# Kernel optimization log

Hardware: AMD Instinct MI355X
Metric: run time of the kernel (lower is better)

## Reference

```python
import jax, jax.numpy as jnp
import numpy as np


def setup_inputs() -> dict:
    key = jax.random.key(0)
    x = jax.random.normal(key, (16384, 4096), dtype=jnp.float32)
    return {"x": x, "k": 64}


def reference(x, k):
    # allow_negative_topk=False -> select and output based on ReLU(x)
    scores = jax.nn.relu(x)                      # [N, D]
    kk = min(k, scores.shape[-1])
    _, topk_idx = jax.lax.top_k(scores, kk)      # [N, kk]
    rows = jnp.arange(scores.shape[0])[:, None]  # [N, 1]
    mask = jnp.zeros_like(scores).at[rows, topk_idx].set(1.0)
    return scores * mask
```

## Files before the change

### kernel.cpp

```cpp
#include <hip/hip_runtime.h>


constexpr int ROW_LEN = 4096;
constexpr int TPB     = 256;
constexpr int SEG     = 128;
constexpr unsigned int KPRE_BITS = 0x3FC00000u;
constexpr unsigned int KMAX_BITS = 0x40C00000u;

typedef float f32x4 __attribute__((ext_vector_type(4)));

__global__ __launch_bounds__(TPB, 4)
void topk_relu_kernel(const float* __restrict__ x, const int* __restrict__ kptr,
                      float* __restrict__ out, int rows)
{
    __shared__ alignas(16) int hist[256];
    __shared__ unsigned int cand[4 * SEG];
    __shared__ int scnt[4];
    __shared__ unsigned int wmax[4];
    __shared__ unsigned int selT;
    __shared__ int selNeed, selAmb;
    __shared__ unsigned long long wtot64[4];
    __shared__ int sel_digit, sel_kk, sel_eq, sel_flag;

    const int row = blockIdx.x;
    if (row >= rows) return;
    const int tid  = threadIdx.x;
    const int lane = tid & 63;
    const int wid  = tid >> 6;

    int k = *kptr;
    if (k > ROW_LEN) k = ROW_LEN;

    const float* __restrict__ xrow = x + (size_t)row * ROW_LEN;
    unsigned int key[16];
#pragma unroll
    for (int j = 0; j < 4; ++j) {
        f32x4 v = *(const f32x4*)(xrow + j * 1024 + tid * 4);
#pragma unroll
        for (int c = 0; c < 4; ++c)
            key[4 * j + c] = __float_as_uint(fmaxf(v[c], 0.0f));
    }

    unsigned int mx = 0u;
#pragma unroll
    for (int j = 0; j < 16; ++j) mx = key[j] > mx ? key[j] : mx;
#pragma unroll
    for (int d = 1; d < 64; d <<= 1) {
        unsigned int o = __shfl_xor(mx, d);
        mx = o > mx ? o : mx;
    }
    int base = 0;
#pragma unroll
    for (int j = 0; j < 16; ++j) {
        const bool p = key[j] > KPRE_BITS;
        const unsigned long long mask = __ballot(p);
        const int prior = __builtin_amdgcn_mbcnt_hi(
            (unsigned int)(mask >> 32),
            __builtin_amdgcn_mbcnt_lo((unsigned int)mask, 0));
        const int idx = base + prior;
        if (p && idx < SEG) cand[(wid << 7) + idx] = key[j] - KPRE_BITS;
        base += (int)__popcll(mask);
    }
    if (lane == 0) { scnt[wid] = base; wmax[wid] = mx; }
    __syncthreads();

    const int c0 = scnt[0], c1 = scnt[1], c2 = scnt[2], c3 = scnt[3];
    const int cnt = c0 + c1 + c2 + c3;
    const bool segok = (c0 <= SEG) & (c1 <= SEG) & (c2 <= SEG) & (c3 <= SEG);
    unsigned int bmax = wmax[0];
    bmax = wmax[1] > bmax ? wmax[1] : bmax;
    bmax = wmax[2] > bmax ? wmax[2] : bmax;
    bmax = wmax[3] > bmax ? wmax[3] : bmax;

    unsigned int T;
    int need, amb;

    if (cnt >= k && segok && bmax < KMAX_BITS) {
        if (wid == 0) {
            const int sc[4] = {c0, c1, c2, c3};
            unsigned int c[8];
#pragma unroll
            for (int i = 0; i < 8; ++i) {
                const int s   = i >> 1;
                const int off = lane + 64 * (i & 1);
                c[i] = (off < sc[s]) ? cand[(s << 7) + off] : 0u;
            }
            int kk = k;
            int eqv = 0;
            unsigned int prefix = 0;
#pragma unroll
            for (int p = 0; p < 3; ++p) {
                const int shift = 16 - 8 * p;
                ((int4*)hist)[lane] = make_int4(0, 0, 0, 0);
#pragma unroll
                for (int i = 0; i < 8; ++i) {
                    const unsigned int ci = c[i];
                    if (ci != 0u && (p == 0 || (ci >> (shift + 8)) == prefix))
                        atomicAdd(&hist[(ci >> shift) & 255u], 1);
                }
                const int4 h = ((const int4*)hist)[lane];
                const int h0 = h.x, h1 = h.y, h2 = h.z, h3 = h.w;
                const int lsum = h0 + h1 + h2 + h3;
                int suf = lsum;
#pragma unroll
                for (int d = 1; d < 64; d <<= 1) {
                    int v = __shfl_down(suf, d);
                    if (lane < 64 - d) suf += v;
                }
                const unsigned long long mm = __ballot(suf >= kk);
                const int L = 63 - __clzll(mm);
                int dig = 0, kkn = 0, eqn = 0;
                if (lane == L) {
                    int cum = suf - lsum;
                    const int hh[4] = {h0, h1, h2, h3};
#pragma unroll
                    for (int b = 3; b >= 0; --b) {
                        if (cum + hh[b] >= kk) { dig = lane * 4 + b; kkn = kk - cum; eqn = hh[b]; break; }
                        cum += hh[b];
                    }
                }
                dig = __shfl(dig, L);
                kk  = __shfl(kkn, L);
                eqv = __shfl(eqn, L);
                prefix = (prefix << 8) | (unsigned int)dig;
            }
            if (lane == 0) {
                selT    = prefix + KPRE_BITS;
                selNeed = kk;
                selAmb  = (eqv != kk);
            }
        }
        __syncthreads();
        T    = selT;
        need = selNeed;
        amb  = selAmb;
    } else {
        int kk = k;
        unsigned int prefix = 0;
        int t0 = 0;
        for (int p = 0; p < 4; ++p) {
            const int shift = 24 - 8 * p;
            hist[tid] = 0;
            if (tid == 0) sel_flag = 0;
            __syncthreads();
#pragma unroll
            for (int j = 0; j < 16; ++j) {
                const unsigned int kj = key[j];
                if (kj != 0u && (p == 0 || (kj >> (shift + 8)) == prefix))
                    atomicAdd(&hist[(kj >> shift) & 255u], 1);
            }
            __syncthreads();
            if (tid < 64) {
                const int b0 = tid * 4;
                const int h0 = hist[b0 + 0], h1 = hist[b0 + 1];
                const int h2 = hist[b0 + 2], h3 = hist[b0 + 3];
                const int lsum = h0 + h1 + h2 + h3;
                int suf = lsum;
#pragma unroll
                for (int d = 1; d < 64; d <<= 1) {
                    int v = __shfl_down(suf, d);
                    if (lane < 64 - d) suf += v;
                }
                const unsigned long long mm = __ballot(suf >= kk);
                if (mm == 0ull) {
                    if (lane == 0) sel_flag = 1;
                } else {
                    const int L = 63 - __clzll(mm);
                    if (lane == L) {
                        int cum = suf - lsum;
                        const int hh[4] = {h0, h1, h2, h3};
#pragma unroll
                        for (int b = 3; b >= 0; --b) {
                            if (cum + hh[b] >= kk) {
                                sel_digit = b0 + b; sel_kk = kk - cum; sel_eq = hh[b]; break;
                            }
                            cum += hh[b];
                        }
                    }
                }
            }
            __syncthreads();
            if (sel_flag) { t0 = 1; break; }
            prefix = (prefix << 8) | (unsigned int)sel_digit;
            kk = sel_kk;
            __syncthreads();
        }
        if (t0) { T = 0u; need = 0; amb = 1; }
        else    { T = prefix; need = kk; amb = (sel_eq != kk); }
    }

    float* __restrict__ orow = out + (size_t)row * ROW_LEN;

    if (!amb) {
#pragma unroll
        for (int j = 0; j < 4; ++j) {
            f32x4 v;
#pragma unroll
            for (int c2 = 0; c2 < 4; ++c2) {
                const unsigned int kj = key[4 * j + c2];
                v[c2] = (kj >= T && T != 0u) ? __uint_as_float(kj) : 0.0f;
            }
            *(f32x4*)(orow + j * 1024 + tid * 4) = v;
        }
    } else {
        unsigned long long packed = 0ull;
#pragma unroll
        for (int j = 0; j < 4; ++j) {
            int e = 0;
#pragma unroll
            for (int c = 0; c < 4; ++c) e += (key[4 * j + c] == T) ? 1 : 0;
            packed |= (unsigned long long)e << (16 * j);
        }
        unsigned long long incp = packed;
#pragma unroll
        for (int d = 1; d < 64; d <<= 1) {
            unsigned long long v = __shfl_up(incp, d);
            if (lane >= d) incp += v;
        }
        if (lane == 63) wtot64[wid] = incp;
        __syncthreads();
        unsigned long long b64 = 0ull;
        for (int w = 0; w < wid; ++w) b64 += wtot64[w];
        const unsigned long long exclp = b64 + incp - packed;
        const unsigned long long t64 = wtot64[0] + wtot64[1] + wtot64[2] + wtot64[3];
        int S[4];
        S[0] = 0;
        S[1] = (int)(t64 & 0xFFFFull);
        S[2] = S[1] + (int)((t64 >> 16) & 0xFFFFull);
        S[3] = S[2] + (int)((t64 >> 32) & 0xFFFFull);
#pragma unroll
        for (int j = 0; j < 4; ++j) {
            int rr = S[j] + (int)((exclp >> (16 * j)) & 0xFFFFull);
            f32x4 v;
#pragma unroll
            for (int c2 = 0; c2 < 4; ++c2) {
                const unsigned int kj = key[4 * j + c2];
                const bool eq = (kj == T);
                const bool keep = (kj > T) || (eq && rr < need);
                v[c2] = keep ? __uint_as_float(kj) : 0.0f;
                rr += eq ? 1 : 0;
            }
            *(f32x4*)(orow + j * 1024 + tid * 4) = v;
        }
    }
}

extern "C" void kernel_launch(void* const* d_in, const int* in_sizes, int n_in,
                              void* d_out, int out_size, void* d_ws, size_t ws_size,
                              hipStream_t stream)
{
    const float* x    = (const float*)d_in[0];
    const int*   kptr = (const int*)d_in[1];
    float*       out  = (float*)d_out;
    const int rows = in_sizes[0] / ROW_LEN;
    topk_relu_kernel<<<rows, TPB, 0, stream>>>(x, kptr, out, rows);
}
```

Before: 101.2 us.

## Process two rows per block with early prefetch and lighter LDS barriers

Each block now handles two rows. Both rows are loaded into registers up front so the second row's global load overlaps the first row's selection. The per-row logic is moved into a device function sharing one LDS struct. __syncthreads is replaced by a custom barrier that waits only on lgkmcnt before s_barrier. The cost is higher register pressure from 32 keys per thread under launch_bounds(256,4), half as many blocks, and a weaker barrier that no longer waits on outstanding global stores.

```diff
diff --git a/kernel.cpp b/kernel.cpp
--- a/kernel.cpp
+++ b/kernel.cpp
@@ -9,38 +9,26 @@
 
 typedef float f32x4 __attribute__((ext_vector_type(4)));
 
-__global__ __launch_bounds__(TPB, 4)
-void topk_relu_kernel(const float* __restrict__ x, const int* __restrict__ kptr,
-                      float* __restrict__ out, int rows)
+__device__ __forceinline__ void bar_lds() {
+    asm volatile("s_waitcnt lgkmcnt(0)" ::: "memory");
+    __builtin_amdgcn_sched_barrier(0);
+    __builtin_amdgcn_s_barrier();
+}
+
+struct Shm {
+    alignas(16) int hist[256];
+    unsigned int cand[4 * SEG];
+    int scnt[4];
+    unsigned int wmax[4];
+    unsigned int selT;
+    int selNeed, selAmb;
+    unsigned long long wtot64[4];
+    int sel_digit, sel_kk, sel_eq, sel_flag;
+};
+
+__device__ __forceinline__ void topk_row(unsigned int (&key)[16], float* __restrict__ orow,
+                                         int k, int tid, int lane, int wid, Shm& s)
 {
-    __shared__ alignas(16) int hist[256];
-    __shared__ unsigned int cand[4 * SEG];
-    __shared__ int scnt[4];
-    __shared__ unsigned int wmax[4];
-    __shared__ unsigned int selT;
-    __shared__ int selNeed, selAmb;
-    __shared__ unsigned long long wtot64[4];
-    __shared__ int sel_digit, sel_kk, sel_eq, sel_flag;
-
-    const int row = blockIdx.x;
-    if (row >= rows) return;
-    const int tid  = threadIdx.x;
-    const int lane = tid & 63;
-    const int wid  = tid >> 6;
-
-    int k = *kptr;
-    if (k > ROW_LEN) k = ROW_LEN;
-
-    const float* __restrict__ xrow = x + (size_t)row * ROW_LEN;
-    unsigned int key[16];
-#pragma unroll
-    for (int j = 0; j < 4; ++j) {
-        f32x4 v = *(const f32x4*)(xrow + j * 1024 + tid * 4);
-#pragma unroll
-        for (int c = 0; c < 4; ++c)
-            key[4 * j + c] = __float_as_uint(fmaxf(v[c], 0.0f));
-    }
-
     unsigned int mx = 0u;
 #pragma unroll
     for (int j = 0; j < 16; ++j) mx = key[j] > mx ? key[j] : mx;
@@ -58,19 +46,19 @@
             (unsigned int)(mask >> 32),
             __builtin_amdgcn_mbcnt_lo((unsigned int)mask, 0));
         const int idx = base + prior;
-        if (p && idx < SEG) cand[(wid << 7) + idx] = key[j] - KPRE_BITS;
+        if (p && idx < SEG) s.cand[(wid << 7) + idx] = key[j] - KPRE_BITS;
         base += (int)__popcll(mask);
     }
-    if (lane == 0) { scnt[wid] = base; wmax[wid] = mx; }
-    __syncthreads();
-
-    const int c0 = scnt[0], c1 = scnt[1], c2 = scnt[2], c3 = scnt[3];
+    if (lane == 0) { s.scnt[wid] = base; s.wmax[wid] = mx; }
+    bar_lds();
+
+    const int c0 = s.scnt[0], c1 = s.scnt[1], c2 = s.scnt[2], c3 = s.scnt[3];
     const int cnt = c0 + c1 + c2 + c3;
     const bool segok = (c0 <= SEG) & (c1 <= SEG) & (c2 <= SEG) & (c3 <= SEG);
-    unsigned int bmax = wmax[0];
-    bmax = wmax[1] > bmax ? wmax[1] : bmax;
-    bmax = wmax[2] > bmax ? wmax[2] : bmax;
-    bmax = wmax[3] > bmax ? wmax[3] : bmax;
+    unsigned int bmax = s.wmax[0];
+    bmax = s.wmax[1] > bmax ? s.wmax[1] : bmax;
+    bmax = s.wmax[2] > bmax ? s.wmax[2] : bmax;
+    bmax = s.wmax[3] > bmax ? s.wmax[3] : bmax;
 
     unsigned int T;
     int need, amb;
@@ -81,9 +69,9 @@
             unsigned int c[8];
 #pragma unroll
             for (int i = 0; i < 8; ++i) {
-                const int s   = i >> 1;
+                const int sgi = i >> 1;
                 const int off = lane + 64 * (i & 1);
-                c[i] = (off < sc[s]) ? cand[(s << 7) + off] : 0u;
+                c[i] = (off < sc[sgi]) ? s.cand[(sgi << 7) + off] : 0u;
             }
             int kk = k;
             int eqv = 0;
@@ -91,14 +79,14 @@
 #pragma unroll
             for (int p = 0; p < 3; ++p) {
                 const int shift = 16 - 8 * p;
-                ((int4*)hist)[lane] = make_int4(0, 0, 0, 0);
+                ((int4*)s.hist)[lane] = make_int4(0, 0, 0, 0);
 #pragma unroll
                 for (int i = 0; i < 8; ++i) {
                     const unsigned int ci = c[i];
                     if (ci != 0u && (p == 0 || (ci >> (shift + 8)) == prefix))
-                        atomicAdd(&hist[(ci >> shift) & 255u], 1);
-                }
-                const int4 h = ((const int4*)hist)[lane];
+                        atomicAdd(&s.hist[(ci >> shift) & 255u], 1);
+                }
+                const int4 h = ((const int4*)s.hist)[lane];
                 const int h0 = h.x, h1 = h.y, h2 = h.z, h3 = h.w;
                 const int lsum = h0 + h1 + h2 + h3;
                 int suf = lsum;
@@ -125,35 +113,35 @@
                 prefix = (prefix << 8) | (unsigned int)dig;
             }
             if (lane == 0) {
-                selT    = prefix + KPRE_BITS;
-                selNeed = kk;
-                selAmb  = (eqv != kk);
-            }
-        }
-        __syncthreads();
-        T    = selT;
-        need = selNeed;
-        amb  = selAmb;
+                s.selT    = prefix + KPRE_BITS;
+                s.selNeed = kk;
+                s.selAmb  = (eqv != kk);
+            }
+        }
+        bar_lds();
+        T    = s.selT;
+        need = s.selNeed;
+        amb  = s.selAmb;
     } else {
         int kk = k;
         unsigned int prefix = 0;
         int t0 = 0;
         for (int p = 0; p < 4; ++p) {
             const int shift = 24 - 8 * p;
-            hist[tid] = 0;
-            if (tid == 0) sel_flag = 0;
-            __syncthreads();
+            s.hist[tid] = 0;
+            if (tid == 0) s.sel_flag = 0;
+            bar_lds();
 #pragma unroll
             for (int j = 0; j < 16; ++j) {
                 const unsigned int kj = key[j];
                 if (kj != 0u && (p == 0 || (kj >> (shift + 8)) == prefix))
-                    atomicAdd(&hist[(kj >> shift) & 255u], 1);
-            }
-            __syncthreads();
+                    atomicAdd(&s.hist[(kj >> shift) & 255u], 1);
+            }
+            bar_lds();
             if (tid < 64) {
                 const int b0 = tid * 4;
-                const int h0 = hist[b0 + 0], h1 = hist[b0 + 1];
-                const int h2 = hist[b0 + 2], h3 = hist[b0 + 3];
+                const int h0 = s.hist[b0 + 0], h1 = s.hist[b0 + 1];
+                const int h2 = s.hist[b0 + 2], h3 = s.hist[b0 + 3];
                 const int lsum = h0 + h1 + h2 + h3;
                 int suf = lsum;
 #pragma unroll
@@ -163,7 +151,7 @@
                 }
                 const unsigned long long mm = __ballot(suf >= kk);
                 if (mm == 0ull) {
-                    if (lane == 0) sel_flag = 1;
+                    if (lane == 0) s.sel_flag = 1;
                 } else {
                     const int L = 63 - __clzll(mm);
                     if (lane == L) {
@@ -172,24 +160,22 @@
 #pragma unroll
                         for (int b = 3; b >= 0; --b) {
                             if (cum + hh[b] >= kk) {
-                                sel_digit = b0 + b; sel_kk = kk - cum; sel_eq = hh[b]; break;
+                                s.sel_digit = b0 + b; s.sel_kk = kk - cum; s.sel_eq = hh[b]; break;
                             }
                             cum += hh[b];
                         }
                     }
                 }
             }
-            __syncthreads();
-            if (sel_flag) { t0 = 1; break; }
-            prefix = (prefix << 8) | (unsigned int)sel_digit;
-            kk = sel_kk;
-            __syncthreads();
+            bar_lds();
+            if (s.sel_flag) { t0 = 1; break; }
+            prefix = (prefix << 8) | (unsigned int)s.sel_digit;
+            kk = s.sel_kk;
+            bar_lds();
         }
         if (t0) { T = 0u; need = 0; amb = 1; }
-        else    { T = prefix; need = kk; amb = (sel_eq != kk); }
-    }
-
-    float* __restrict__ orow = out + (size_t)row * ROW_LEN;
+        else    { T = prefix; need = kk; amb = (s.sel_eq != kk); }
+    }
 
     if (!amb) {
 #pragma unroll
@@ -217,12 +203,12 @@
             unsigned long long v = __shfl_up(incp, d);
             if (lane >= d) incp += v;
         }
-        if (lane == 63) wtot64[wid] = incp;
-        __syncthreads();
+        if (lane == 63) s.wtot64[wid] = incp;
+        bar_lds();
         unsigned long long b64 = 0ull;
-        for (int w = 0; w < wid; ++w) b64 += wtot64[w];
+        for (int w = 0; w < wid; ++w) b64 += s.wtot64[w];
         const unsigned long long exclp = b64 + incp - packed;
-        const unsigned long long t64 = wtot64[0] + wtot64[1] + wtot64[2] + wtot64[3];
+        const unsigned long long t64 = s.wtot64[0] + s.wtot64[1] + s.wtot64[2] + s.wtot64[3];
         int S[4];
         S[0] = 0;
         S[1] = (int)(t64 & 0xFFFFull);
@@ -242,6 +228,52 @@
             }
             *(f32x4*)(orow + j * 1024 + tid * 4) = v;
         }
+    }
+}
+
+__global__ __launch_bounds__(TPB, 4)
+void topk_relu_kernel(const float* __restrict__ x, const int* __restrict__ kptr,
+                      float* __restrict__ out, int rows)
+{
+    __shared__ Shm s;
+
+    const int tid  = threadIdx.x;
+    const int lane = tid & 63;
+    const int wid  = tid >> 6;
+
+    const int rowA = blockIdx.x * 2;
+    const int rowB = rowA + 1;
+    if (rowA >= rows) return;
+
+    int k = *kptr;
+    if (k > ROW_LEN) k = ROW_LEN;
+
+    const float* __restrict__ xrowA = x + (size_t)rowA * ROW_LEN;
+    unsigned int keyA[16];
+#pragma unroll
+    for (int j = 0; j < 4; ++j) {
+        f32x4 v = *(const f32x4*)(xrowA + j * 1024 + tid * 4);
+#pragma unroll
+        for (int c = 0; c < 4; ++c)
+            keyA[4 * j + c] = __float_as_uint(fmaxf(v[c], 0.0f));
+    }
+    const bool haveB = (rowB < rows);
+    unsigned int keyB[16];
+    if (haveB) {
+        const float* __restrict__ xrowB = x + (size_t)rowB * ROW_LEN;
+#pragma unroll
+        for (int j = 0; j < 4; ++j) {
+            f32x4 v = *(const f32x4*)(xrowB + j * 1024 + tid * 4);
+#pragma unroll
+            for (int c = 0; c < 4; ++c)
+                keyB[4 * j + c] = __float_as_uint(fmaxf(v[c], 0.0f));
+        }
+    }
+
+    topk_row(keyA, out + (size_t)rowA * ROW_LEN, k, tid, lane, wid, s);
+    if (haveB) {
+        bar_lds();
+        topk_row(keyB, out + (size_t)rowB * ROW_LEN, k, tid, lane, wid, s);
     }
 }
 
@@ -253,5 +285,6 @@
     const int*   kptr = (const int*)d_in[1];
     float*       out  = (float*)d_out;
     const int rows = in_sizes[0] / ROW_LEN;
-    topk_relu_kernel<<<rows, TPB, 0, stream>>>(x, kptr, out, rows);
-}
+    const int nb = (rows + 1) / 2;
+    topk_relu_kernel<<<nb, TPB, 0, stream>>>(x, kptr, out, rows);
+}
```

After: 107.1 us. +5.8%, slower.
